# Performance work log

Hardware: AMD Instinct MI355X
Metric: run time of the kernel (lower is better)

## Reference

```python
import jax, jax.numpy as jnp
import numpy as np

N_NODES = 100000
N_EDGES = 1600000
D_IN = 64
D_OUT = 64


def setup_inputs() -> dict:
    key = jax.random.key(0)
    k1, k2, k3, k4 = jax.random.split(key, 4)
    x = jax.random.normal(k1, (N_NODES, D_IN), dtype=jnp.float32)
    edge_index = jax.random.randint(k2, (2, N_EDGES), 0, N_NODES, dtype=jnp.int64)
    W = jax.random.normal(k3, (D_OUT, D_IN), dtype=jnp.float32) * (1.0 / np.sqrt(D_IN))
    b = jax.random.normal(k4, (D_OUT,), dtype=jnp.float32) * 0.01
    return {"x": x, "edge_index": edge_index, "W": W, "b": b}


def reference(x, edge_index, W, b):
    num_nodes = x.shape[0]
    row, col = edge_index[0], edge_index[1]
    # degree of each node as a destination (scatter_add of ones over row)
    deg = jax.ops.segment_sum(jnp.ones(row.shape[0], dtype=x.dtype), row,
                              num_segments=num_nodes)
    # deg^-0.5 with inf (deg==0) replaced by 0
    deg_inv_sqrt = jnp.where(deg > 0, jax.lax.rsqrt(jnp.maximum(deg, 1.0)) * jnp.where(deg > 0, 1.0, 0.0), 0.0)
    deg_inv_sqrt = jnp.where(deg > 0, deg ** -0.5, 0.0)
    # gather source features, scale by source norm, scatter-add to destinations
    weighted = x[col] * deg_inv_sqrt[col][:, None]          # [E, D_IN]
    agg = jax.ops.segment_sum(weighted, row, num_segments=num_nodes)  # [N, D_IN]
    agg = agg * deg_inv_sqrt[:, None]
    # linear + relu (torch Linear: y = agg @ W.T + b)
    return jax.nn.relu(agg @ W.T + b)
```

## Files before the change

kernel.cpp:

```cpp
#include <hip/hip_runtime.h>

#define N_NODES 100000
#define N_EDGES 1600000
#define D 64

#define BSHIFT 6
#define BNODES 64
#define NBUCKET 1563
#define CAP 1408
#define CHUNK 4096
#define EPT 16
#define NCHUNK 391
#define COLBITS 17
#define COLMASK 0x1FFFF

#define BCUR_OFF  0
#define PAIRS_OFF 8192
#define Y_OFF     8811008

__device__ __forceinline__ float bf2f(unsigned short u) {
    return __uint_as_float(((unsigned)u) << 16);
}
__device__ __forceinline__ unsigned f2bf(float f) {
    unsigned bits = __float_as_uint(f);
    return (bits + 0x7FFFu + ((bits >> 16) & 1u)) >> 16;
}

__global__ void initcur_kernel(int* __restrict__ bcur) {
    int i = blockIdx.x * blockDim.x + threadIdx.x;
    if (i < NBUCKET) bcur[i] = i * CAP;
}

__global__ __launch_bounds__(256) void scat_kernel(const int* __restrict__ row,
                                                   const int* __restrict__ col,
                                                   int* __restrict__ bcur,
                                                   int* __restrict__ pairs) {
    __shared__ int lcnt[NBUCKET];
    int t = threadIdx.x;
    int base = blockIdx.x * CHUNK;
    for (int i = t; i < NBUCKET; i += 256) lcnt[i] = 0;
    __syncthreads();
    int r[EPT], c[EPT], pos[EPT];
#pragma unroll
    for (int i = 0; i < EPT; ++i) {
        int e = base + i * 256 + t;
        if (e < N_EDGES) {
            r[i] = row[e];
            c[i] = col[e];
            pos[i] = atomicAdd(&lcnt[r[i] >> BSHIFT], 1);
        } else r[i] = -1;
    }
    __syncthreads();
    for (int i = t; i < NBUCKET; i += 256) {
        int cc = lcnt[i];
        if (cc) lcnt[i] = atomicAdd(&bcur[i], cc);
    }
    __syncthreads();
#pragma unroll
    for (int i = 0; i < EPT; ++i) {
        if (r[i] >= 0) {
            int b = r[i] >> BSHIFT;
            int rl = r[i] & (BNODES - 1);
            pairs[lcnt[b] + pos[i]] = (rl << COLBITS) | c[i];
        }
    }
}

__global__ __launch_bounds__(256) void xform_kernel(
        const float* __restrict__ x, const float* __restrict__ W,
        const int* __restrict__ pairs, const int* __restrict__ bcur,
        unsigned short* __restrict__ y) {
    __shared__ __align__(16) float XT[D * 68];
    __shared__ __align__(16) float WT[D * 68];
    __shared__ int hist[BNODES];
    __shared__ float dl[BNODES];
    int t = threadIdx.x;
    int b = blockIdx.x;
    int nb0 = b << BSHIFT;
    for (int i = t; i < D * D; i += 256) {
        int j = i >> 6, d = i & 63;
        WT[d * 68 + j] = W[i];
    }
    if (t < BNODES) hist[t] = 0;
    __syncthreads();
    for (int i = t; i < BNODES * D; i += 256) {
        int n = i >> 6, d = i & 63;
        int g = nb0 + n;
        XT[d * 68 + n] = (g < N_NODES) ? x[(size_t)g * D + d] : 0.0f;
    }
    int beg = b * CAP, end = bcur[b];
    for (int k = beg + t; k < end; k += 256)
        atomicAdd(&hist[pairs[k] >> COLBITS], 1);
    __syncthreads();
    if (t < BNODES) dl[t] = (hist[t] > 0) ? rsqrtf((float)hist[t]) : 0.0f;
    __syncthreads();
    int tj = t & 15, tn = t >> 4;
    float4 a0 = {0,0,0,0}, a1 = {0,0,0,0}, a2 = {0,0,0,0}, a3 = {0,0,0,0};
#pragma unroll 8
    for (int d = 0; d < D; ++d) {
        float4 xv = *(const float4*)&XT[d * 68 + tn * 4];
        float4 wv = *(const float4*)&WT[d * 68 + tj * 4];
        a0.x = fmaf(xv.x, wv.x, a0.x); a0.y = fmaf(xv.x, wv.y, a0.y);
        a0.z = fmaf(xv.x, wv.z, a0.z); a0.w = fmaf(xv.x, wv.w, a0.w);
        a1.x = fmaf(xv.y, wv.x, a1.x); a1.y = fmaf(xv.y, wv.y, a1.y);
        a1.z = fmaf(xv.y, wv.z, a1.z); a1.w = fmaf(xv.y, wv.w, a1.w);
        a2.x = fmaf(xv.z, wv.x, a2.x); a2.y = fmaf(xv.z, wv.y, a2.y);
        a2.z = fmaf(xv.z, wv.z, a2.z); a2.w = fmaf(xv.z, wv.w, a2.w);
        a3.x = fmaf(xv.w, wv.x, a3.x); a3.y = fmaf(xv.w, wv.y, a3.y);
        a3.z = fmaf(xv.w, wv.z, a3.z); a3.w = fmaf(xv.w, wv.w, a3.w);
    }
    int jb = tj * 4;
    {
        int g = nb0 + tn * 4;
        if (g < N_NODES) {
            float s = dl[tn * 4];
            unsigned lo = f2bf(a0.x * s) | (f2bf(a0.y * s) << 16);
            unsigned hi = f2bf(a0.z * s) | (f2bf(a0.w * s) << 16);
            *(uint2*)(y + (size_t)g * D + jb) = make_uint2(lo, hi);
        }
    }
    {
        int g = nb0 + tn * 4 + 1;
        if (g < N_NODES) {
            float s = dl[tn * 4 + 1];
            unsigned lo = f2bf(a1.x * s) | (f2bf(a1.y * s) << 16);
            unsigned hi = f2bf(a1.z * s) | (f2bf(a1.w * s) << 16);
            *(uint2*)(y + (size_t)g * D + jb) = make_uint2(lo, hi);
        }
    }
    {
        int g = nb0 + tn * 4 + 2;
        if (g < N_NODES) {
            float s = dl[tn * 4 + 2];
            unsigned lo = f2bf(a2.x * s) | (f2bf(a2.y * s) << 16);
            unsigned hi = f2bf(a2.z * s) | (f2bf(a2.w * s) << 16);
            *(uint2*)(y + (size_t)g * D + jb) = make_uint2(lo, hi);
        }
    }
    {
        int g = nb0 + tn * 4 + 3;
        if (g < N_NODES) {
            float s = dl[tn * 4 + 3];
            unsigned lo = f2bf(a3.x * s) | (f2bf(a3.y * s) << 16);
            unsigned hi = f2bf(a3.z * s) | (f2bf(a3.w * s) << 16);
            *(uint2*)(y + (size_t)g * D + jb) = make_uint2(lo, hi);
        }
    }
}

__global__ __launch_bounds__(256) void mega_kernel(
        const int* __restrict__ pairs, const int* __restrict__ bcur,
        const unsigned short* __restrict__ y,
        const float* __restrict__ bias, float* __restrict__ out) {
    __shared__ int hist[BNODES];
    __shared__ int sc[BNODES];
    __shared__ int lrptr[BNODES + 1];
    __shared__ int lcur[BNODES];
    __shared__ float dl[BNODES];
    __shared__ int lds_scol[CAP];
    int t = threadIdx.x;
    int b = blockIdx.x;
    int beg = b * CAP, end = bcur[b];
    if (t < BNODES) hist[t] = 0;
    __syncthreads();
    for (int k = beg + t; k < end; k += 256)
        atomicAdd(&hist[pairs[k] >> COLBITS], 1);
    __syncthreads();
    if (t < BNODES) sc[t] = hist[t];
    __syncthreads();
    for (int off = 1; off < BNODES; off <<= 1) {
        int v = (t < BNODES && t >= off) ? sc[t - off] : 0;
        __syncthreads();
        if (t < BNODES) sc[t] += v;
        __syncthreads();
    }
    if (t < BNODES) {
        lrptr[t + 1] = sc[t];
        lcur[t] = sc[t] - hist[t];
        dl[t] = (hist[t] > 0) ? rsqrtf((float)hist[t]) : 0.0f;
    }
    if (t == 0) lrptr[0] = 0;
    __syncthreads();
    for (int k = beg + t; k < end; k += 256) {
        int p = pairs[k];
        int pos = atomicAdd(&lcur[p >> COLBITS], 1);
        lds_scol[pos] = p & COLMASK;
    }
    __syncthreads();
    int wave = t >> 6, j = t & 63;
    float bj = bias[j];
    for (int ln = wave; ln < BNODES; ln += 4) {
        int n = (b << BSHIFT) + ln;
        if (n >= N_NODES) break;
        int s = lrptr[ln], e2 = lrptr[ln + 1];
        float a0 = 0, a1 = 0, a2 = 0, a3 = 0, a4 = 0, a5 = 0, a6 = 0, a7 = 0;
        int k = s;
        for (; k + 7 < e2; k += 8) {
            int c0 = lds_scol[k + 0], c1 = lds_scol[k + 1];
            int c2 = lds_scol[k + 2], c3 = lds_scol[k + 3];
            int c4 = lds_scol[k + 4], c5 = lds_scol[k + 5];
            int c6 = lds_scol[k + 6], c7 = lds_scol[k + 7];
            a0 += bf2f(y[(size_t)c0 * D + j]);
            a1 += bf2f(y[(size_t)c1 * D + j]);
            a2 += bf2f(y[(size_t)c2 * D + j]);
            a3 += bf2f(y[(size_t)c3 * D + j]);
            a4 += bf2f(y[(size_t)c4 * D + j]);
            a5 += bf2f(y[(size_t)c5 * D + j]);
            a6 += bf2f(y[(size_t)c6 * D + j]);
            a7 += bf2f(y[(size_t)c7 * D + j]);
        }
        for (; k < e2; ++k) a0 += bf2f(y[(size_t)lds_scol[k] * D + j]);
        float sum = ((a0 + a1) + (a2 + a3)) + ((a4 + a5) + (a6 + a7));
        out[(size_t)n * D + j] = fmaxf(fmaf(dl[ln], sum, bj), 0.0f);
    }
}

extern "C" void kernel_launch(void* const* d_in, const int* in_sizes, int n_in,
                              void* d_out, int out_size, void* d_ws, size_t ws_size,
                              hipStream_t stream) {
    const float* x    = (const float*)d_in[0];
    const int*   eidx = (const int*)d_in[1];
    const float* W    = (const float*)d_in[2];
    const float* b    = (const float*)d_in[3];
    float* out = (float*)d_out;
    char* ws = (char*)d_ws;

    const int* row = eidx;
    const int* col = eidx + N_EDGES;

    int* bcur  = (int*)(ws + BCUR_OFF);
    int* pairs = (int*)(ws + PAIRS_OFF);
    unsigned short* y = (unsigned short*)(ws + Y_OFF);

    initcur_kernel<<<(NBUCKET + 255) / 256, 256, 0, stream>>>(bcur);
    scat_kernel<<<NCHUNK, 256, 0, stream>>>(row, col, bcur, pairs);
    xform_kernel<<<NBUCKET, 256, 0, stream>>>(x, W, pairs, bcur, y);
    mega_kernel<<<NBUCKET, 256, 0, stream>>>(pairs, bcur, y, b, out);
}
```

Measured before the change: 185.5 us.

## Replace single-pass bucket scatter with two-level coarse/fine radix bucketing

The edge binning becomes two passes. The first scatters edges into 49 coarse buckets of 2048 destination rows with few shared atomics. The second refines each coarse bucket into 32-node fine buckets, so global scatter writes are more localized and shared counters are small. The aggregation kernel now runs on 32-node buckets for more blocks and smaller LDS. This adds an extra kernel launch and an extra read/write pass over all edge pairs.

```diff
diff --git a/kernel.cpp b/kernel.cpp
--- a/kernel.cpp
+++ b/kernel.cpp
@@ -4,19 +4,29 @@
 #define N_EDGES 1600000
 #define D 64
 
-#define BSHIFT 6
-#define BNODES 64
-#define NBUCKET 1563
-#define CAP 1408
+#define FSHIFT 5
+#define FNODES 32
+#define NFB 3125
+#define CAPF 800
+
+#define CSHIFT 11
+#define NCB 49
+#define CCAP 36864
+#define FPC 64
+#define NCHUNKB 9
+
 #define CHUNK 4096
 #define EPT 16
-#define NCHUNK 391
+#define NCHUNKA 391
+
 #define COLBITS 17
 #define COLMASK 0x1FFFF
 
-#define BCUR_OFF  0
-#define PAIRS_OFF 8192
-#define Y_OFF     8811008
+#define FCUR_OFF   0
+#define CCUR_OFF   16384
+#define CPAIRS_OFF 32768
+#define FPAIRS_OFF 7258112
+#define Y_OFF      17258112
 
 __device__ __forceinline__ float bf2f(unsigned short u) {
     return __uint_as_float(((unsigned)u) << 16);
@@ -26,19 +36,20 @@
     return (bits + 0x7FFFu + ((bits >> 16) & 1u)) >> 16;
 }
 
-__global__ void initcur_kernel(int* __restrict__ bcur) {
+__global__ void initcur_kernel(int* __restrict__ fcur, int* __restrict__ ccur) {
     int i = blockIdx.x * blockDim.x + threadIdx.x;
-    if (i < NBUCKET) bcur[i] = i * CAP;
-}
-
-__global__ __launch_bounds__(256) void scat_kernel(const int* __restrict__ row,
-                                                   const int* __restrict__ col,
-                                                   int* __restrict__ bcur,
-                                                   int* __restrict__ pairs) {
-    __shared__ int lcnt[NBUCKET];
+    if (i < NFB) fcur[i] = i * CAPF;
+    if (i < NCB) ccur[i] = i * CCAP;
+}
+
+__global__ __launch_bounds__(256) void scatA_kernel(const int* __restrict__ row,
+                                                    const int* __restrict__ col,
+                                                    int* __restrict__ ccur,
+                                                    int* __restrict__ cpairs) {
+    __shared__ int lcnt[NCB];
     int t = threadIdx.x;
     int base = blockIdx.x * CHUNK;
-    for (int i = t; i < NBUCKET; i += 256) lcnt[i] = 0;
+    if (t < NCB) lcnt[t] = 0;
     __syncthreads();
     int r[EPT], c[EPT], pos[EPT];
 #pragma unroll
@@ -47,52 +58,96 @@
         if (e < N_EDGES) {
             r[i] = row[e];
             c[i] = col[e];
-            pos[i] = atomicAdd(&lcnt[r[i] >> BSHIFT], 1);
+            pos[i] = atomicAdd(&lcnt[r[i] >> CSHIFT], 1);
         } else r[i] = -1;
     }
     __syncthreads();
-    for (int i = t; i < NBUCKET; i += 256) {
-        int cc = lcnt[i];
-        if (cc) lcnt[i] = atomicAdd(&bcur[i], cc);
+    if (t < NCB) {
+        int cc = lcnt[t];
+        if (cc) lcnt[t] = atomicAdd(&ccur[t], cc);
     }
     __syncthreads();
 #pragma unroll
     for (int i = 0; i < EPT; ++i) {
         if (r[i] >= 0) {
-            int b = r[i] >> BSHIFT;
-            int rl = r[i] & (BNODES - 1);
-            pairs[lcnt[b] + pos[i]] = (rl << COLBITS) | c[i];
+            int cb = r[i] >> CSHIFT;
+            int rl = r[i] & ((1 << CSHIFT) - 1);
+            cpairs[lcnt[cb] + pos[i]] = (rl << COLBITS) | c[i];
+        }
+    }
+}
+
+__global__ __launch_bounds__(256) void scatB_kernel(const int* __restrict__ cpairs,
+                                                    const int* __restrict__ ccur,
+                                                    int* __restrict__ fcur,
+                                                    int* __restrict__ fpairs) {
+    __shared__ int lcnt[FPC];
+    int t = threadIdx.x;
+    int cb = blockIdx.x / NCHUNKB;
+    int k  = blockIdx.x % NCHUNKB;
+    int beg = cb * CCAP + k * CHUNK;
+    int end = ccur[cb];
+    if (end > beg + CHUNK) end = beg + CHUNK;
+    if (t < FPC) lcnt[t] = 0;
+    __syncthreads();
+    int pc[EPT], pos[EPT];
+#pragma unroll
+    for (int i = 0; i < EPT; ++i) {
+        int e = beg + i * 256 + t;
+        if (e < end) {
+            pc[i] = cpairs[e];
+            pos[i] = atomicAdd(&lcnt[pc[i] >> (COLBITS + FSHIFT)], 1);
+        } else pc[i] = -1;
+    }
+    __syncthreads();
+    if (t < FPC) {
+        int cc = lcnt[t];
+        if (cc) lcnt[t] = atomicAdd(&fcur[(cb << 6) + t], cc);
+    }
+    __syncthreads();
+#pragma unroll
+    for (int i = 0; i < EPT; ++i) {
+        if (pc[i] >= 0) {
+            int fl = pc[i] >> (COLBITS + FSHIFT);
+            int rl5 = (pc[i] >> COLBITS) & (FNODES - 1);
+            fpairs[lcnt[fl] + pos[i]] = (rl5 << COLBITS) | (pc[i] & COLMASK);
         }
     }
 }
 
 __global__ __launch_bounds__(256) void xform_kernel(
         const float* __restrict__ x, const float* __restrict__ W,
-        const int* __restrict__ pairs, const int* __restrict__ bcur,
+        const int* __restrict__ fpairs, const int* __restrict__ fcur,
         unsigned short* __restrict__ y) {
     __shared__ __align__(16) float XT[D * 68];
     __shared__ __align__(16) float WT[D * 68];
-    __shared__ int hist[BNODES];
-    __shared__ float dl[BNODES];
+    __shared__ int hist[64];
+    __shared__ float dl[64];
     int t = threadIdx.x;
     int b = blockIdx.x;
-    int nb0 = b << BSHIFT;
+    int nb0 = b << 6;
     for (int i = t; i < D * D; i += 256) {
         int j = i >> 6, d = i & 63;
         WT[d * 68 + j] = W[i];
     }
-    if (t < BNODES) hist[t] = 0;
-    __syncthreads();
-    for (int i = t; i < BNODES * D; i += 256) {
+    if (t < 64) hist[t] = 0;
+    __syncthreads();
+    for (int i = t; i < 64 * D; i += 256) {
         int n = i >> 6, d = i & 63;
         int g = nb0 + n;
         XT[d * 68 + n] = (g < N_NODES) ? x[(size_t)g * D + d] : 0.0f;
     }
-    int beg = b * CAP, end = bcur[b];
-    for (int k = beg + t; k < end; k += 256)
-        atomicAdd(&hist[pairs[k] >> COLBITS], 1);
-    __syncthreads();
-    if (t < BNODES) dl[t] = (hist[t] > 0) ? rsqrtf((float)hist[t]) : 0.0f;
+#pragma unroll
+    for (int half = 0; half < 2; ++half) {
+        int f = 2 * b + half;
+        if (f < NFB) {
+            int beg = f * CAPF, end = fcur[f];
+            for (int k = beg + t; k < end; k += 256)
+                atomicAdd(&hist[(fpairs[k] >> COLBITS) + (half << FSHIFT)], 1);
+        }
+    }
+    __syncthreads();
+    if (t < 64) dl[t] = (hist[t] > 0) ? rsqrtf((float)hist[t]) : 0.0f;
     __syncthreads();
     int tj = t & 15, tn = t >> 4;
     float4 a0 = {0,0,0,0}, a1 = {0,0,0,0}, a2 = {0,0,0,0}, a3 = {0,0,0,0};
@@ -110,71 +165,46 @@
         a3.z = fmaf(xv.w, wv.z, a3.z); a3.w = fmaf(xv.w, wv.w, a3.w);
     }
     int jb = tj * 4;
-    {
-        int g = nb0 + tn * 4;
+#pragma unroll
+    for (int s = 0; s < 4; ++s) {
+        int g = nb0 + tn * 4 + s;
         if (g < N_NODES) {
-            float s = dl[tn * 4];
-            unsigned lo = f2bf(a0.x * s) | (f2bf(a0.y * s) << 16);
-            unsigned hi = f2bf(a0.z * s) | (f2bf(a0.w * s) << 16);
+            float sc = dl[tn * 4 + s];
+            float4 a = (s == 0) ? a0 : (s == 1) ? a1 : (s == 2) ? a2 : a3;
+            unsigned lo = f2bf(a.x * sc) | (f2bf(a.y * sc) << 16);
+            unsigned hi = f2bf(a.z * sc) | (f2bf(a.w * sc) << 16);
             *(uint2*)(y + (size_t)g * D + jb) = make_uint2(lo, hi);
         }
     }
-    {
-        int g = nb0 + tn * 4 + 1;
-        if (g < N_NODES) {
-            float s = dl[tn * 4 + 1];
-            unsigned lo = f2bf(a1.x * s) | (f2bf(a1.y * s) << 16);
-            unsigned hi = f2bf(a1.z * s) | (f2bf(a1.w * s) << 16);
-            *(uint2*)(y + (size_t)g * D + jb) = make_uint2(lo, hi);
-        }
-    }
-    {
-        int g = nb0 + tn * 4 + 2;
-        if (g < N_NODES) {
-            float s = dl[tn * 4 + 2];
-            unsigned lo = f2bf(a2.x * s) | (f2bf(a2.y * s) << 16);
-            unsigned hi = f2bf(a2.z * s) | (f2bf(a2.w * s) << 16);
-            *(uint2*)(y + (size_t)g * D + jb) = make_uint2(lo, hi);
-        }
-    }
-    {
-        int g = nb0 + tn * 4 + 3;
-        if (g < N_NODES) {
-            float s = dl[tn * 4 + 3];
-            unsigned lo = f2bf(a3.x * s) | (f2bf(a3.y * s) << 16);
-            unsigned hi = f2bf(a3.z * s) | (f2bf(a3.w * s) << 16);
-            *(uint2*)(y + (size_t)g * D + jb) = make_uint2(lo, hi);
-        }
-    }
 }
 
 __global__ __launch_bounds__(256) void mega_kernel(
-        const int* __restrict__ pairs, const int* __restrict__ bcur,
+        const int* __restrict__ fpairs, const int* __restrict__ fcur,
         const unsigned short* __restrict__ y,
         const float* __restrict__ bias, float* __restrict__ out) {
-    __shared__ int hist[BNODES];
-    __shared__ int sc[BNODES];
-    __shared__ int lrptr[BNODES + 1];
-    __shared__ int lcur[BNODES];
-    __shared__ float dl[BNODES];
-    __shared__ int lds_scol[CAP];
+    __shared__ int hist[FNODES];
+    __shared__ int sc[FNODES];
+    __shared__ int lrptr[FNODES + 1];
+    __shared__ int lcur[FNODES];
+    __shared__ float dl[FNODES];
+    __shared__ int lds_scol[CAPF];
     int t = threadIdx.x;
     int b = blockIdx.x;
-    int beg = b * CAP, end = bcur[b];
-    if (t < BNODES) hist[t] = 0;
+    int beg = b * CAPF, end = fcur[b];
+    if (t < FNODES) hist[t] = 0;
     __syncthreads();
     for (int k = beg + t; k < end; k += 256)
-        atomicAdd(&hist[pairs[k] >> COLBITS], 1);
-    __syncthreads();
-    if (t < BNODES) sc[t] = hist[t];
-    __syncthreads();
-    for (int off = 1; off < BNODES; off <<= 1) {
-        int v = (t < BNODES && t >= off) ? sc[t - off] : 0;
+        atomicAdd(&hist[fpairs[k] >> COLBITS], 1);
+    __syncthreads();
+    if (t < FNODES) sc[t] = hist[t];
+    __syncthreads();
+    for (int off = 1; off < FNODES; off <<= 1) {
+        int v = (t < FNODES && t >= off) ? sc[t - off] : 0;
         __syncthreads();
-        if (t < BNODES) sc[t] += v;
+        if (t < FNODES) sc[t] += v;
         __syncthreads();
     }
-    if (t < BNODES) {
+    if (t < FNODES) {
         lrptr[t + 1] = sc[t];
         lcur[t] = sc[t] - hist[t];
         dl[t] = (hist[t] > 0) ? rsqrtf((float)hist[t]) : 0.0f;
@@ -182,16 +212,14 @@
     if (t == 0) lrptr[0] = 0;
     __syncthreads();
     for (int k = beg + t; k < end; k += 256) {
-        int p = pairs[k];
+        int p = fpairs[k];
         int pos = atomicAdd(&lcur[p >> COLBITS], 1);
         lds_scol[pos] = p & COLMASK;
     }
     __syncthreads();
     int wave = t >> 6, j = t & 63;
     float bj = bias[j];
-    for (int ln = wave; ln < BNODES; ln += 4) {
-        int n = (b << BSHIFT) + ln;
-        if (n >= N_NODES) break;
+    for (int ln = wave; ln < FNODES; ln += 4) {
         int s = lrptr[ln], e2 = lrptr[ln + 1];
         float a0 = 0, a1 = 0, a2 = 0, a3 = 0, a4 = 0, a5 = 0, a6 = 0, a7 = 0;
         int k = s;
@@ -211,6 +239,7 @@
         }
         for (; k < e2; ++k) a0 += bf2f(y[(size_t)lds_scol[k] * D + j]);
         float sum = ((a0 + a1) + (a2 + a3)) + ((a4 + a5) + (a6 + a7));
+        int n = (b << FSHIFT) + ln;
         out[(size_t)n * D + j] = fmaxf(fmaf(dl[ln], sum, bj), 0.0f);
     }
 }
@@ -228,12 +257,15 @@
     const int* row = eidx;
     const int* col = eidx + N_EDGES;
 
-    int* bcur  = (int*)(ws + BCUR_OFF);
-    int* pairs = (int*)(ws + PAIRS_OFF);
+    int* fcur   = (int*)(ws + FCUR_OFF);
+    int* ccur   = (int*)(ws + CCUR_OFF);
+    int* cpairs = (int*)(ws + CPAIRS_OFF);
+    int* fpairs = (int*)(ws + FPAIRS_OFF);
     unsigned short* y = (unsigned short*)(ws + Y_OFF);
 
-    initcur_kernel<<<(NBUCKET + 255) / 256, 256, 0, stream>>>(bcur);
-    scat_kernel<<<NCHUNK, 256, 0, stream>>>(row, col, bcur, pairs);
-    xform_kernel<<<NBUCKET, 256, 0, stream>>>(x, W, pairs, bcur, y);
-    mega_kernel<<<NBUCKET, 256, 0, stream>>>(pairs, bcur, y, b, out);
-}
+    initcur_kernel<<<(NFB + 255) / 256, 256, 0, stream>>>(fcur, ccur);
+    scatA_kernel<<<NCHUNKA, 256, 0, stream>>>(row, col, ccur, cpairs);
+    scatB_kernel<<<NCB * NCHUNKB, 256, 0, stream>>>(cpairs, ccur, fcur, fpairs);
+    xform_kernel<<<(N_NODES + 63) / 64, 256, 0, stream>>>(x, W, fpairs, fcur, y);
+    mega_kernel<<<NFB, 256, 0, stream>>>(fpairs, fcur, y, b, out);
+}
```

After: 189.8 us. 1.02x slower.
